# Kernel tuning notes

Hardware: AMD Instinct MI355X
Metric: run time of the kernel (lower is better)

## Reference

```python
import jax, jax.numpy as jnp
import numpy as np

B = 2048      # number of scenes (samples)
A = 64        # max agents per scene
D = 128       # latent_size (embed dim)
H = 4         # heads (hardcoded in module)
HD = D // H   # head dim = 32
NEG = -1e9


def setup_inputs() -> dict:
    key = jax.random.key(0)
    k1, k2, k3, k4 = jax.random.split(key, 4)
    # flat ragged agent features; only the first sum(agents) rows are 'real'
    att_in = jax.random.normal(k1, (B * A, D), dtype=jnp.float32)
    agents_per_sample = jax.random.randint(k2, (B,), 1, A + 1)  # each scene has >=1 agent
    s = 1.0 / np.sqrt(D)
    w_in = jax.random.uniform(k3, (3 * D, D), minval=-s, maxval=s, dtype=jnp.float32)
    b_in = jnp.zeros((3 * D,), dtype=jnp.float32)
    w_out = jax.random.uniform(k4, (D, D), minval=-s, maxval=s, dtype=jnp.float32)
    b_out = jnp.zeros((D,), dtype=jnp.float32)
    return {"att_in": att_in, "w_in": w_in, "b_in": b_in,
            "w_out": w_out, "b_out": b_out, "agents_per_sample": agents_per_sample}


def reference(att_in, w_in, b_in, w_out, b_out, agents_per_sample):
    # scatter flat ragged rows into padded [B, A, D] (same as padded_att_in[mask] = att_in)
    offsets = jnp.cumsum(agents_per_sample) - agents_per_sample          # exclusive prefix sum
    idx = offsets[:, None] + jnp.arange(A)[None, :]                      # [B, A] flat row index
    mask = jnp.arange(A)[None, :] < agents_per_sample[:, None]          # [B, A] valid-agent mask
    padded = jnp.take(att_in, idx, axis=0) * mask[..., None].astype(att_in.dtype)
    # fused in-projection (nn.MultiheadAttention in_proj)
    qkv = padded @ w_in.T + b_in                                        # [B, A, 3D]
    q, k, v = jnp.split(qkv, 3, axis=-1)
    q = q.reshape(B, A, H, HD)
    k = k.reshape(B, A, H, HD)
    v = v.reshape(B, A, H, HD)
    scores = jnp.einsum('bqhd,bkhd->bhqk', q, k) / np.sqrt(HD).astype(q.dtype)
    # key_padding_mask: padded keys excluded from softmax
    scores = jnp.where(mask[:, None, None, :], scores, NEG)
    attn = jax.nn.softmax(scores, axis=-1)
    ctx = jnp.einsum('bhqk,bkhd->bqhd', attn, v).reshape(B, A, D)
    out = (ctx @ w_out.T + b_out) * mask[..., None].astype(ctx.dtype)   # zero out padded rows (torch slices them off)
    return out
```

## Files before the change

### kernel.cpp

```cpp
#include <hip/hip_runtime.h>
#include <hip/hip_bf16.h>

typedef __bf16 bf16;
typedef __bf16 bf16x4 __attribute__((ext_vector_type(4)));
typedef __bf16 bf16x8 __attribute__((ext_vector_type(8)));
typedef float  f32x4  __attribute__((ext_vector_type(4)));

#define NEG_INF (-1e9f)
#define N_SCENES 2048

__global__ __launch_bounds__(256) void prep_kernel(
    const float* __restrict__ w_in, const float* __restrict__ w_out,
    const int* __restrict__ agents,
    bf16* __restrict__ w_in_b, bf16* __restrict__ w_out_b, int* __restrict__ offs)
{
    __shared__ int tot[256];
    const int t = threadIdx.x;
    if (blockIdx.x == 0) {
        int loc[8]; int s = 0;
        #pragma unroll
        for (int j = 0; j < 8; ++j) { loc[j] = agents[t * 8 + j]; s += loc[j]; }
        tot[t] = s;
        __syncthreads();
        for (int o = 1; o < 256; o <<= 1) {
            int v = (t >= o) ? tot[t - o] : 0;
            __syncthreads();
            tot[t] += v;
            __syncthreads();
        }
        int run = tot[t] - s;
        #pragma unroll
        for (int j = 0; j < 8; ++j) { offs[t * 8 + j] = run; run += loc[j]; }
    } else {
        int i = (blockIdx.x - 1) * 1024 + t * 4;
        float4 v; bf16* dst;
        if (i < 49152) { v = *(const float4*)(w_in + i);            dst = w_in_b + i; }
        else           { v = *(const float4*)(w_out + (i - 49152)); dst = w_out_b + (i - 49152); }
        bf16x4 o = { (bf16)v.x, (bf16)v.y, (bf16)v.z, (bf16)v.w };
        *(bf16x4*)dst = o;
    }
}

__global__ __launch_bounds__(256, 3) void attn_kernel(
    const float* __restrict__ att_in,
    const float* __restrict__ b_in, const float* __restrict__ b_out,
    const bf16* __restrict__ w_in_b, const bf16* __restrict__ w_out_b,
    const int* __restrict__ agents, const int* __restrict__ offs,
    float* __restrict__ out)
{
    __shared__ bf16 s_lds[4 * 6144];

    const int b    = blockIdx.x;
    const int tid  = threadIdx.x;
    const int lane = tid & 63;
    const int w    = tid >> 6;
    const int h    = w;
    const int r    = lane & 15;
    const int qd   = lane >> 4;
    const int r7   = lane & 7;
    const int nb   = agents[b];
    const int off  = offs[b];
    const int mtc  = (nb + 15) >> 4;
    const int mt16 = mtc << 4;

    bf16* qk = s_lds + w * 6144;
    bf16* vT = qk + 4096;

    {
        const float4 z4 = make_float4(0.f, 0.f, 0.f, 0.f);
        const int nz = (64 - mt16) * 32;
        for (int i = tid; i < nz; i += 256) {
            int row = mt16 + (i >> 5);
            *(float4*)(out + ((size_t)b * 64 + row) * 128 + (i & 31) * 4) = z4;
        }
    }

    if (mtc & 1) {
        int row = lane >> 1, half = lane & 1;
        int c = (2 * mtc + half) ^ (row & 7);
        bf16x8 z8 = {(bf16)0.f,(bf16)0.f,(bf16)0.f,(bf16)0.f,
                     (bf16)0.f,(bf16)0.f,(bf16)0.f,(bf16)0.f};
        *(bf16x8*)(vT + row * 64 + c * 8) = z8;
    }

    bf16x8 xa[4][4];
    #pragma unroll
    for (int mt = 0; mt < 4; ++mt)
        #pragma unroll
        for (int ks = 0; ks < 4; ++ks) {
            float4 lo = make_float4(0.f,0.f,0.f,0.f), hi = lo;
            int row = mt * 16 + r;
            if (row < nb) {
                const float* p = att_in + (((size_t)(off + row)) << 7) + ks * 32 + qd * 8;
                lo = *(const float4*)p;
                hi = *(const float4*)(p + 4);
            }
            xa[mt][ks] = (bf16x8){(bf16)lo.x,(bf16)lo.y,(bf16)lo.z,(bf16)lo.w,
                                  (bf16)hi.x,(bf16)hi.y,(bf16)hi.z,(bf16)hi.w};
        }

    #pragma unroll
    for (int t = 0; t < 6; ++t) {
        const int kind = t >> 1, sub = t & 1;
        const int j0 = kind * 128 + h * 32 + sub * 16;
        bf16x8 wb[4];
        #pragma unroll
        for (int ks = 0; ks < 4; ++ks)
            wb[ks] = *(const bf16x8*)(w_in_b + (size_t)(j0 + r) * 128 + ks * 32 + qd * 8);
        const float bias = b_in[j0 + r];
        #pragma unroll
        for (int mt = 0; mt < 4; ++mt) {
            if (mt < mtc) {
                f32x4 acc = {0.f, 0.f, 0.f, 0.f};
                #pragma unroll
                for (int ks = 0; ks < 4; ++ks)
                    acc = __builtin_amdgcn_mfma_f32_16x16x32_bf16(xa[mt][ks], wb[ks], acc, 0, 0, 0);
                if (kind < 2) {
                    int chunk = kind * 4 + sub * 2 + (r >> 3);
                    #pragma unroll
                    for (int i = 0; i < 4; ++i) {
                        int row = mt * 16 + qd * 4 + i;
                        int c = chunk ^ (row & 7);
                        qk[row * 64 + c * 8 + r7] = (bf16)(acc[i] + bias);
                    }
                } else {
                    int row = sub * 16 + r;
                    int c = (2 * mt + (qd >> 1)) ^ r7;
                    bf16x4 pk = {(bf16)(acc[0]+bias), (bf16)(acc[1]+bias),
                                 (bf16)(acc[2]+bias), (bf16)(acc[3]+bias)};
                    *(bf16x4*)(vT + row * 64 + c * 8 + (qd & 1) * 4) = pk;
                }
            }
        }
    }

    bf16x8 qa[4], kb[4];
    #pragma unroll
    for (int mt = 0; mt < 4; ++mt)
        if (mt < mtc) {
            int row = mt * 16 + r;
            qa[mt] = *(const bf16x8*)(qk + row * 64 + ((qd) ^ r7) * 8);
            kb[mt] = *(const bf16x8*)(qk + row * 64 + ((4 + qd) ^ r7) * 8);
        }
    f32x4 S[4][4];
    #pragma unroll
    for (int mt = 0; mt < 4; ++mt)
        if (mt < mtc)
            #pragma unroll
            for (int nt = 0; nt < 4; ++nt)
                if (nt < mtc) {
                    f32x4 z = {0.f, 0.f, 0.f, 0.f};
                    S[mt][nt] = __builtin_amdgcn_mfma_f32_16x16x32_bf16(qa[mt], kb[nt], z, 0, 0, 0);
                }

    const float scale = 0.17677669529663687f;
    bool kvalid[4];
    #pragma unroll
    for (int nt = 0; nt < 4; ++nt) kvalid[nt] = (nt < mtc) && ((nt * 16 + r) < nb);
    #pragma unroll
    for (int mt = 0; mt < 4; ++mt)
        if (mt < mtc)
            #pragma unroll
            for (int i = 0; i < 4; ++i) {
                float v[4]; float mx = NEG_INF;
                #pragma unroll
                for (int nt = 0; nt < 4; ++nt) {
                    float val = kvalid[nt] ? S[mt][nt][i] * scale : NEG_INF;
                    v[nt] = val; mx = fmaxf(mx, val);
                }
                mx = fmaxf(mx, __shfl_xor(mx, 1));
                mx = fmaxf(mx, __shfl_xor(mx, 2));
                mx = fmaxf(mx, __shfl_xor(mx, 4));
                mx = fmaxf(mx, __shfl_xor(mx, 8));
                float l = 0.f;
                #pragma unroll
                for (int nt = 0; nt < 4; ++nt) { v[nt] = __expf(v[nt] - mx); l += v[nt]; }
                l += __shfl_xor(l, 1); l += __shfl_xor(l, 2);
                l += __shfl_xor(l, 4); l += __shfl_xor(l, 8);
                float rl = 1.0f / l;
                #pragma unroll
                for (int nt = 0; nt < 4; ++nt) S[mt][nt][i] = v[nt] * rl;
            }

    f32x4 cacc[4][2];
    #pragma unroll
    for (int mt = 0; mt < 4; ++mt)
        #pragma unroll
        for (int n2 = 0; n2 < 2; ++n2)
            cacc[mt][n2] = (f32x4){0.f, 0.f, 0.f, 0.f};
    const int hkc = (mtc + 1) >> 1;
    #pragma unroll
    for (int hk = 0; hk < 2; ++hk)
        if (hk < hkc) {
            #pragma unroll
            for (int mt = 0; mt < 4; ++mt)
                if (mt < mtc)
                    #pragma unroll
                    for (int n2 = 0; n2 < 2; ++n2) {
                        int chunk = 4 + n2 * 2 + (r >> 3);
                        #pragma unroll
                        for (int i = 0; i < 4; ++i) {
                            int row = mt * 16 + qd * 4 + i;
                            int c = chunk ^ (row & 7);
                            qk[row * 64 + c * 8 + r7] = (bf16)S[mt][hk * 2 + n2][i];
                        }
                    }
            bf16x8 vb[2];
            #pragma unroll
            for (int n2 = 0; n2 < 2; ++n2) {
                int row = n2 * 16 + r;
                int c = (hk * 4 + qd) ^ r7;
                vb[n2] = *(const bf16x8*)(vT + row * 64 + c * 8);
            }
            #pragma unroll
            for (int mt = 0; mt < 4; ++mt)
                if (mt < mtc) {
                    int row = mt * 16 + r;
                    bf16x8 pa = *(const bf16x8*)(qk + row * 64 + ((4 + qd) ^ r7) * 8);
                    cacc[mt][0] = __builtin_amdgcn_mfma_f32_16x16x32_bf16(pa, vb[0], cacc[mt][0], 0, 0, 0);
                    cacc[mt][1] = __builtin_amdgcn_mfma_f32_16x16x32_bf16(pa, vb[1], cacc[mt][1], 0, 0, 0);
                }
        }

    #pragma unroll
    for (int mt = 0; mt < 4; ++mt)
        if (mt < mtc)
            #pragma unroll
            for (int n2 = 0; n2 < 2; ++n2) {
                int chunk = n2 * 2 + (r >> 3);
                #pragma unroll
                for (int i = 0; i < 4; ++i) {
                    int row = mt * 16 + qd * 4 + i;
                    int c = chunk ^ (row & 7);
                    qk[row * 64 + c * 8 + r7] = (bf16)cacc[mt][n2][i];
                }
            }
    __syncthreads();

    #pragma unroll
    for (int t2 = 0; t2 < 2; ++t2) {
        const int j0 = (w * 2 + t2) * 16;
        bf16x8 wo[4];
        #pragma unroll
        for (int ks = 0; ks < 4; ++ks)
            wo[ks] = *(const bf16x8*)(w_out_b + (size_t)(j0 + r) * 128 + ks * 32 + qd * 8);
        const float bias = b_out[j0 + r];
        #pragma unroll
        for (int mt = 0; mt < 4; ++mt)
            if (mt < mtc) {
                f32x4 acc = {0.f, 0.f, 0.f, 0.f};
                #pragma unroll
                for (int ks = 0; ks < 4; ++ks) {
                    int row = mt * 16 + r;
                    bf16x8 ca = *(const bf16x8*)(s_lds + ks * 6144 + row * 64 + (qd ^ r7) * 8);
                    acc = __builtin_amdgcn_mfma_f32_16x16x32_bf16(ca, wo[ks], acc, 0, 0, 0);
                }
                #pragma unroll
                for (int i = 0; i < 4; ++i) {
                    int row = mt * 16 + qd * 4 + i;
                    float val = (row < nb) ? (acc[i] + bias) : 0.f;
                    out[((size_t)b * 64 + row) * 128 + j0 + r] = val;
                }
            }
    }
}

extern "C" void kernel_launch(void* const* d_in, const int* in_sizes, int n_in,
                              void* d_out, int out_size, void* d_ws, size_t ws_size,
                              hipStream_t stream)
{
    const float* att_in = (const float*)d_in[0];
    const float* w_in   = (const float*)d_in[1];
    const float* b_in   = (const float*)d_in[2];
    const float* w_out  = (const float*)d_in[3];
    const float* b_out  = (const float*)d_in[4];
    const int*   agents = (const int*)d_in[5];

    bf16* w_in_b  = (bf16*)d_ws;
    bf16* w_out_b = w_in_b + 49152;
    int*  offs    = (int*)((char*)d_ws + 98304 + 32768);

    prep_kernel<<<65, 256, 0, stream>>>(w_in, w_out, agents, w_in_b, w_out_b, offs);
    attn_kernel<<<N_SCENES, 256, 0, stream>>>(att_in, b_in, b_out, w_in_b, w_out_b,
                                              agents, offs, (float*)d_out);
}
```

Baseline: 180.4 us.

## Restructure attention kernel to loop over row tiles and cut register pressure

The fully unrolled per-tile arrays (xa[4][4], S[4][4], cacc[4][2]) become runtime loops over the valid 16-row tiles. Each tile now runs its projection, scores, softmax and PV products in turn, so only one tile's data is held in registers at a time. Weight fragments for the in-projection are reloaded per row tile, and K/V and out-projection weights are hoisted and kept in registers. The aim is lower VGPR use for higher occupancy, at the cost of extra weight loads and less instruction-level parallelism across tiles.

```diff
diff --git a/kernel.cpp b/kernel.cpp
--- a/kernel.cpp
+++ b/kernel.cpp
@@ -76,192 +76,171 @@
     }
 
     if (mtc & 1) {
-        int row = lane >> 1, half = lane & 1;
-        int c = (2 * mtc + half) ^ (row & 7);
+        int zr = lane >> 1, half = lane & 1;
+        int c = (2 * mtc + half) ^ (zr & 7);
         bf16x8 z8 = {(bf16)0.f,(bf16)0.f,(bf16)0.f,(bf16)0.f,
                      (bf16)0.f,(bf16)0.f,(bf16)0.f,(bf16)0.f};
-        *(bf16x8*)(vT + row * 64 + c * 8) = z8;
-    }
-
-    bf16x8 xa[4][4];
-    #pragma unroll
-    for (int mt = 0; mt < 4; ++mt)
+        *(bf16x8*)(vT + zr * 64 + c * 8) = z8;
+    }
+
+    for (int mt = 0; mt < mtc; ++mt) {
+        const int xrow = mt * 16 + r;
+        const bool vr = xrow < nb;
+        const float* px = att_in + (((size_t)(off + xrow)) << 7) + qd * 8;
+        bf16x8 xa[4];
         #pragma unroll
         for (int ks = 0; ks < 4; ++ks) {
             float4 lo = make_float4(0.f,0.f,0.f,0.f), hi = lo;
-            int row = mt * 16 + r;
-            if (row < nb) {
-                const float* p = att_in + (((size_t)(off + row)) << 7) + ks * 32 + qd * 8;
-                lo = *(const float4*)p;
-                hi = *(const float4*)(p + 4);
-            }
-            xa[mt][ks] = (bf16x8){(bf16)lo.x,(bf16)lo.y,(bf16)lo.z,(bf16)lo.w,
-                                  (bf16)hi.x,(bf16)hi.y,(bf16)hi.z,(bf16)hi.w};
-        }
-
-    #pragma unroll
-    for (int t = 0; t < 6; ++t) {
-        const int kind = t >> 1, sub = t & 1;
-        const int j0 = kind * 128 + h * 32 + sub * 16;
-        bf16x8 wb[4];
-        #pragma unroll
-        for (int ks = 0; ks < 4; ++ks)
-            wb[ks] = *(const bf16x8*)(w_in_b + (size_t)(j0 + r) * 128 + ks * 32 + qd * 8);
-        const float bias = b_in[j0 + r];
-        #pragma unroll
-        for (int mt = 0; mt < 4; ++mt) {
-            if (mt < mtc) {
-                f32x4 acc = {0.f, 0.f, 0.f, 0.f};
+            if (vr) {
+                lo = *(const float4*)(px + ks * 32);
+                hi = *(const float4*)(px + ks * 32 + 4);
+            }
+            xa[ks] = (bf16x8){(bf16)lo.x,(bf16)lo.y,(bf16)lo.z,(bf16)lo.w,
+                              (bf16)hi.x,(bf16)hi.y,(bf16)hi.z,(bf16)hi.w};
+        }
+        #pragma unroll
+        for (int t = 0; t < 6; ++t) {
+            const int kind = t >> 1, sub = t & 1;
+            const int j0 = kind * 128 + h * 32 + sub * 16;
+            const bf16* pw = w_in_b + (size_t)(j0 + r) * 128 + qd * 8;
+            bf16x8 wb[4];
+            #pragma unroll
+            for (int ks = 0; ks < 4; ++ks)
+                wb[ks] = *(const bf16x8*)(pw + ks * 32);
+            const float bias = b_in[j0 + r];
+            f32x4 acc = {0.f, 0.f, 0.f, 0.f};
+            #pragma unroll
+            for (int ks = 0; ks < 4; ++ks)
+                acc = __builtin_amdgcn_mfma_f32_16x16x32_bf16(xa[ks], wb[ks], acc, 0, 0, 0);
+            if (kind < 2) {
+                const int chunk = kind * 4 + sub * 2 + (r >> 3);
                 #pragma unroll
-                for (int ks = 0; ks < 4; ++ks)
-                    acc = __builtin_amdgcn_mfma_f32_16x16x32_bf16(xa[mt][ks], wb[ks], acc, 0, 0, 0);
-                if (kind < 2) {
-                    int chunk = kind * 4 + sub * 2 + (r >> 3);
-                    #pragma unroll
-                    for (int i = 0; i < 4; ++i) {
-                        int row = mt * 16 + qd * 4 + i;
-                        int c = chunk ^ (row & 7);
-                        qk[row * 64 + c * 8 + r7] = (bf16)(acc[i] + bias);
-                    }
-                } else {
-                    int row = sub * 16 + r;
-                    int c = (2 * mt + (qd >> 1)) ^ r7;
-                    bf16x4 pk = {(bf16)(acc[0]+bias), (bf16)(acc[1]+bias),
-                                 (bf16)(acc[2]+bias), (bf16)(acc[3]+bias)};
-                    *(bf16x4*)(vT + row * 64 + c * 8 + (qd & 1) * 4) = pk;
+                for (int i = 0; i < 4; ++i) {
+                    int row2 = mt * 16 + qd * 4 + i;
+                    int c = chunk ^ (row2 & 7);
+                    qk[row2 * 64 + c * 8 + r7] = (bf16)(acc[i] + bias);
                 }
-            }
-        }
-    }
-
-    bf16x8 qa[4], kb[4];
-    #pragma unroll
-    for (int mt = 0; mt < 4; ++mt)
-        if (mt < mtc) {
-            int row = mt * 16 + r;
-            qa[mt] = *(const bf16x8*)(qk + row * 64 + ((qd) ^ r7) * 8);
-            kb[mt] = *(const bf16x8*)(qk + row * 64 + ((4 + qd) ^ r7) * 8);
-        }
-    f32x4 S[4][4];
-    #pragma unroll
-    for (int mt = 0; mt < 4; ++mt)
-        if (mt < mtc)
-            #pragma unroll
-            for (int nt = 0; nt < 4; ++nt)
-                if (nt < mtc) {
-                    f32x4 z = {0.f, 0.f, 0.f, 0.f};
-                    S[mt][nt] = __builtin_amdgcn_mfma_f32_16x16x32_bf16(qa[mt], kb[nt], z, 0, 0, 0);
-                }
-
+            } else {
+                const int vrow = sub * 16 + r;
+                const int c = (2 * mt + (qd >> 1)) ^ r7;
+                bf16x4 pk = {(bf16)(acc[0]+bias), (bf16)(acc[1]+bias),
+                             (bf16)(acc[2]+bias), (bf16)(acc[3]+bias)};
+                *(bf16x4*)(vT + vrow * 64 + c * 8 + (qd & 1) * 4) = pk;
+            }
+        }
+    }
+
+    bf16x8 kb[4];
+    #pragma unroll
+    for (int nt = 0; nt < 4; ++nt) {
+        int row = nt * 16 + r;
+        kb[nt] = *(const bf16x8*)(qk + row * 64 + ((4 + qd) ^ r7) * 8);
+    }
+    bf16x8 vb[2][2];
+    #pragma unroll
+    for (int hk = 0; hk < 2; ++hk)
+        #pragma unroll
+        for (int n2 = 0; n2 < 2; ++n2) {
+            int row = n2 * 16 + r;
+            vb[hk][n2] = *(const bf16x8*)(vT + row * 64 + ((hk * 4 + qd) ^ r7) * 8);
+        }
+    const int hkc = (mtc + 1) >> 1;
     const float scale = 0.17677669529663687f;
     bool kvalid[4];
     #pragma unroll
     for (int nt = 0; nt < 4; ++nt) kvalid[nt] = (nt < mtc) && ((nt * 16 + r) < nb);
-    #pragma unroll
-    for (int mt = 0; mt < 4; ++mt)
-        if (mt < mtc)
-            #pragma unroll
-            for (int i = 0; i < 4; ++i) {
-                float v[4]; float mx = NEG_INF;
-                #pragma unroll
-                for (int nt = 0; nt < 4; ++nt) {
-                    float val = kvalid[nt] ? S[mt][nt][i] * scale : NEG_INF;
-                    v[nt] = val; mx = fmaxf(mx, val);
-                }
-                mx = fmaxf(mx, __shfl_xor(mx, 1));
-                mx = fmaxf(mx, __shfl_xor(mx, 2));
-                mx = fmaxf(mx, __shfl_xor(mx, 4));
-                mx = fmaxf(mx, __shfl_xor(mx, 8));
-                float l = 0.f;
-                #pragma unroll
-                for (int nt = 0; nt < 4; ++nt) { v[nt] = __expf(v[nt] - mx); l += v[nt]; }
-                l += __shfl_xor(l, 1); l += __shfl_xor(l, 2);
-                l += __shfl_xor(l, 4); l += __shfl_xor(l, 8);
-                float rl = 1.0f / l;
-                #pragma unroll
-                for (int nt = 0; nt < 4; ++nt) S[mt][nt][i] = v[nt] * rl;
-            }
-
-    f32x4 cacc[4][2];
-    #pragma unroll
-    for (int mt = 0; mt < 4; ++mt)
-        #pragma unroll
-        for (int n2 = 0; n2 < 2; ++n2)
-            cacc[mt][n2] = (f32x4){0.f, 0.f, 0.f, 0.f};
-    const int hkc = (mtc + 1) >> 1;
-    #pragma unroll
-    for (int hk = 0; hk < 2; ++hk)
-        if (hk < hkc) {
-            #pragma unroll
-            for (int mt = 0; mt < 4; ++mt)
-                if (mt < mtc)
-                    #pragma unroll
-                    for (int n2 = 0; n2 < 2; ++n2) {
-                        int chunk = 4 + n2 * 2 + (r >> 3);
-                        #pragma unroll
-                        for (int i = 0; i < 4; ++i) {
-                            int row = mt * 16 + qd * 4 + i;
-                            int c = chunk ^ (row & 7);
-                            qk[row * 64 + c * 8 + r7] = (bf16)S[mt][hk * 2 + n2][i];
-                        }
-                    }
-            bf16x8 vb[2];
+
+    for (int mt = 0; mt < mtc; ++mt) {
+        const int arow = mt * 16 + r;
+        const bf16x8 qa = *(const bf16x8*)(qk + arow * 64 + (qd ^ r7) * 8);
+        f32x4 S[4];
+        #pragma unroll
+        for (int nt = 0; nt < 4; ++nt)
+            if (nt < mtc) {
+                f32x4 z = {0.f, 0.f, 0.f, 0.f};
+                S[nt] = __builtin_amdgcn_mfma_f32_16x16x32_bf16(qa, kb[nt], z, 0, 0, 0);
+            }
+        #pragma unroll
+        for (int i = 0; i < 4; ++i) {
+            float v[4]; float mx = NEG_INF;
+            #pragma unroll
+            for (int nt = 0; nt < 4; ++nt) {
+                float val = kvalid[nt] ? S[nt][i] * scale : NEG_INF;
+                v[nt] = val; mx = fmaxf(mx, val);
+            }
+            mx = fmaxf(mx, __shfl_xor(mx, 1));
+            mx = fmaxf(mx, __shfl_xor(mx, 2));
+            mx = fmaxf(mx, __shfl_xor(mx, 4));
+            mx = fmaxf(mx, __shfl_xor(mx, 8));
+            float l = 0.f;
+            #pragma unroll
+            for (int nt = 0; nt < 4; ++nt) { v[nt] = __expf(v[nt] - mx); l += v[nt]; }
+            l += __shfl_xor(l, 1); l += __shfl_xor(l, 2);
+            l += __shfl_xor(l, 4); l += __shfl_xor(l, 8);
+            float rl = 1.0f / l;
+            #pragma unroll
+            for (int nt = 0; nt < 4; ++nt) S[nt][i] = v[nt] * rl;
+        }
+        f32x4 c0 = {0.f,0.f,0.f,0.f}, c1 = {0.f,0.f,0.f,0.f};
+        for (int hk = 0; hk < hkc; ++hk) {
             #pragma unroll
             for (int n2 = 0; n2 < 2; ++n2) {
-                int row = n2 * 16 + r;
-                int c = (hk * 4 + qd) ^ r7;
-                vb[n2] = *(const bf16x8*)(vT + row * 64 + c * 8);
-            }
-            #pragma unroll
-            for (int mt = 0; mt < 4; ++mt)
-                if (mt < mtc) {
-                    int row = mt * 16 + r;
-                    bf16x8 pa = *(const bf16x8*)(qk + row * 64 + ((4 + qd) ^ r7) * 8);
-                    cacc[mt][0] = __builtin_amdgcn_mfma_f32_16x16x32_bf16(pa, vb[0], cacc[mt][0], 0, 0, 0);
-                    cacc[mt][1] = __builtin_amdgcn_mfma_f32_16x16x32_bf16(pa, vb[1], cacc[mt][1], 0, 0, 0);
-                }
-        }
-
-    #pragma unroll
-    for (int mt = 0; mt < 4; ++mt)
-        if (mt < mtc)
-            #pragma unroll
-            for (int n2 = 0; n2 < 2; ++n2) {
-                int chunk = n2 * 2 + (r >> 3);
+                const int chunk = 4 + n2 * 2 + (r >> 3);
                 #pragma unroll
                 for (int i = 0; i < 4; ++i) {
-                    int row = mt * 16 + qd * 4 + i;
-                    int c = chunk ^ (row & 7);
-                    qk[row * 64 + c * 8 + r7] = (bf16)cacc[mt][n2][i];
+                    int row2 = mt * 16 + qd * 4 + i;
+                    int c = chunk ^ (row2 & 7);
+                    qk[row2 * 64 + c * 8 + r7] = (bf16)S[hk * 2 + n2][i];
                 }
             }
+            const bf16x8 pa = *(const bf16x8*)(qk + arow * 64 + ((4 + qd) ^ r7) * 8);
+            c0 = __builtin_amdgcn_mfma_f32_16x16x32_bf16(pa, vb[hk][0], c0, 0, 0, 0);
+            c1 = __builtin_amdgcn_mfma_f32_16x16x32_bf16(pa, vb[hk][1], c1, 0, 0, 0);
+        }
+        #pragma unroll
+        for (int n2 = 0; n2 < 2; ++n2) {
+            const int chunk = n2 * 2 + (r >> 3);
+            const f32x4 cc = n2 ? c1 : c0;
+            #pragma unroll
+            for (int i = 0; i < 4; ++i) {
+                int row2 = mt * 16 + qd * 4 + i;
+                int c = chunk ^ (row2 & 7);
+                qk[row2 * 64 + c * 8 + r7] = (bf16)cc[i];
+            }
+        }
+    }
     __syncthreads();
 
+    bf16x8 wo[2][4]; float ob[2];
     #pragma unroll
     for (int t2 = 0; t2 < 2; ++t2) {
         const int j0 = (w * 2 + t2) * 16;
-        bf16x8 wo[4];
+        const bf16* pw = w_out_b + (size_t)(j0 + r) * 128 + qd * 8;
         #pragma unroll
         for (int ks = 0; ks < 4; ++ks)
-            wo[ks] = *(const bf16x8*)(w_out_b + (size_t)(j0 + r) * 128 + ks * 32 + qd * 8);
-        const float bias = b_out[j0 + r];
-        #pragma unroll
-        for (int mt = 0; mt < 4; ++mt)
-            if (mt < mtc) {
-                f32x4 acc = {0.f, 0.f, 0.f, 0.f};
-                #pragma unroll
-                for (int ks = 0; ks < 4; ++ks) {
-                    int row = mt * 16 + r;
-                    bf16x8 ca = *(const bf16x8*)(s_lds + ks * 6144 + row * 64 + (qd ^ r7) * 8);
-                    acc = __builtin_amdgcn_mfma_f32_16x16x32_bf16(ca, wo[ks], acc, 0, 0, 0);
-                }
-                #pragma unroll
-                for (int i = 0; i < 4; ++i) {
-                    int row = mt * 16 + qd * 4 + i;
-                    float val = (row < nb) ? (acc[i] + bias) : 0.f;
-                    out[((size_t)b * 64 + row) * 128 + j0 + r] = val;
-                }
-            }
+            wo[t2][ks] = *(const bf16x8*)(pw + ks * 32);
+        ob[t2] = b_out[j0 + r];
+    }
+    for (int mt = 0; mt < mtc; ++mt) {
+        const int arow = mt * 16 + r;
+        bf16x8 ca[4];
+        #pragma unroll
+        for (int ks = 0; ks < 4; ++ks)
+            ca[ks] = *(const bf16x8*)(s_lds + ks * 6144 + arow * 64 + (qd ^ r7) * 8);
+        #pragma unroll
+        for (int t2 = 0; t2 < 2; ++t2) {
+            f32x4 acc = {0.f, 0.f, 0.f, 0.f};
+            #pragma unroll
+            for (int ks = 0; ks < 4; ++ks)
+                acc = __builtin_amdgcn_mfma_f32_16x16x32_bf16(ca[ks], wo[t2][ks], acc, 0, 0, 0);
+            const int j0 = (w * 2 + t2) * 16;
+            #pragma unroll
+            for (int i = 0; i < 4; ++i) {
+                int row2 = mt * 16 + qd * 4 + i;
+                float val = (row2 < nb) ? (acc[i] + ob[t2]) : 0.f;
+                out[((size_t)b * 64 + row2) * 128 + j0 + r] = val;
+            }
+        }
     }
 }
 
```

Result: slower. 298.5 us (+65.4%).
